# Kernel optimization log

Measured on AMD Instinct MI355X. Metric: run time of the kernel, lower is better.

Reference implementation:

```python
import jax, jax.numpy as jnp
import numpy as np

N_NODES = 50000
NUM_LAYERS = 3


def setup_inputs() -> dict:
    key = jax.random.key(0)
    k1, k2, k3, k4, k5, k6 = jax.random.split(key, 6)
    E = 800000
    IN, OUT = 64, 64
    src = jax.random.randint(k1, (E,), 0, N_NODES)
    dst = jax.random.randint(k2, (E,), 0, N_NODES)
    edge_index = jnp.stack([src, dst], axis=0)  # [2, E]
    edge_weight = jax.random.uniform(k3, (E,), dtype=jnp.float32)
    H = jax.random.normal(k4, (N_NODES, IN), dtype=jnp.float32)
    W = jax.random.normal(k5, (IN, OUT), dtype=jnp.float32) * (1.0 / np.sqrt(IN))
    b = jax.random.normal(k6, (OUT,), dtype=jnp.float32) * 0.01
    return {"edge_index": edge_index, "edge_weight": edge_weight, "H": H, "W": W, "b": b}


def _spmm(edge_index, edge_weight, H):
    # out[dst] += w * H[src]  (sparse A @ H)
    src, dst = edge_index[0], edge_index[1]
    msgs = edge_weight[:, None] * H[src]            # [E, d]
    return jax.ops.segment_sum(msgs, dst, num_segments=N_NODES)


def reference(edge_index, edge_weight, H, W, b):
    for _ in range(NUM_LAYERS):
        H = _spmm(edge_index, edge_weight, H)
    return H @ W + b  # nn.Linear
```

## Files before the change

### kernel.cpp

```cpp
#include <hip/hip_runtime.h>
#include <hip/hip_fp16.h>

#define N_NODES 50000
#define NFEAT 64
#define NB_BUCKETS ((N_NODES + 255) / 256)
#define CHUNK 4096

#define FMA4(A, S, V)                                                          \
    do {                                                                       \
        A.x = fmaf(S, V.x, A.x);                                               \
        A.y = fmaf(S, V.y, A.y);                                               \
        A.z = fmaf(S, V.z, A.z);                                               \
        A.w = fmaf(S, V.w, A.w);                                               \
    } while (0)


__global__ __launch_bounds__(256) void k_bhist(const int* __restrict__ dst, int E,
                                               int* __restrict__ bucketCount) {
    __shared__ int cnt[NB_BUCKETS];
    for (int i = threadIdx.x; i < NB_BUCKETS; i += 256) cnt[i] = 0;
    __syncthreads();
    int cbeg = blockIdx.x * CHUNK;
    int cend = min(cbeg + CHUNK, E);
    for (int e = cbeg + threadIdx.x; e < cend; e += 256)
        atomicAdd(&cnt[dst[e] >> 8], 1);
    __syncthreads();
    for (int i = threadIdx.x; i < NB_BUCKETS; i += 256)
        if (cnt[i]) atomicAdd(&bucketCount[i], cnt[i]);
}

__global__ __launch_bounds__(256) void k_bscan(const int* __restrict__ bucketCount,
                                               int E, int* __restrict__ bucketBase,
                                               int* __restrict__ bucketCursor,
                                               int* __restrict__ offs) {
    __shared__ int s[256];
    int t = threadIdx.x;
    int v = (t < NB_BUCKETS) ? bucketCount[t] : 0;
    s[t] = v;
    __syncthreads();
    for (int off = 1; off < 256; off <<= 1) {
        int u = (t >= off) ? s[t - off] : 0;
        __syncthreads();
        if (t >= off) s[t] += u;
        __syncthreads();
    }
    if (t < NB_BUCKETS) {
        int b = s[t] - v;
        bucketBase[t] = b;
        bucketCursor[t] = b;
    }
    if (t == 0) {
        bucketBase[NB_BUCKETS] = E;
        offs[N_NODES] = E;
    }
}

__global__ __launch_bounds__(256) void k_bplace(const int* __restrict__ src,
                                                const int* __restrict__ dst,
                                                const float* __restrict__ w, int E,
                                                int* __restrict__ bucketCursor,
                                                int2* __restrict__ tmp) {
    __shared__ int cnt[NB_BUCKETS];
    __shared__ int base[NB_BUCKETS];
    for (int i = threadIdx.x; i < NB_BUCKETS; i += 256) cnt[i] = 0;
    __syncthreads();
    int cbeg = blockIdx.x * CHUNK;
    int cend = min(cbeg + CHUNK, E);
    for (int e = cbeg + threadIdx.x; e < cend; e += 256)
        atomicAdd(&cnt[dst[e] >> 8], 1);
    __syncthreads();
    for (int i = threadIdx.x; i < NB_BUCKETS; i += 256) {
        int c = cnt[i];
        base[i] = c ? atomicAdd(&bucketCursor[i], c) : 0;
        cnt[i] = 0;
    }
    __syncthreads();
    for (int e = cbeg + threadIdx.x; e < cend; e += 256) {
        int d = dst[e];
        int b = d >> 8;
        int r = atomicAdd(&cnt[b], 1);
        tmp[base[b] + r] = make_int2(((d & 255) << 16) | src[e], __float_as_int(w[e]));
    }
}

__global__ __launch_bounds__(256) void k_bsort(const int* __restrict__ bucketBase,
                                               const int2* __restrict__ tmp,
                                               int2* __restrict__ pairs,
                                               int* __restrict__ offs) {
    __shared__ int cnt[256];
    __shared__ int ex[256];
    int b = blockIdx.x;
    int t = threadIdx.x;
    int beg = bucketBase[b], end = bucketBase[b + 1];
    cnt[t] = 0;
    __syncthreads();
    for (int e = beg + t; e < end; e += 256)
        atomicAdd(&cnt[(tmp[e].x >> 16) & 255], 1);
    __syncthreads();
    int v = cnt[t];
    ex[t] = v;
    __syncthreads();
    for (int off = 1; off < 256; off <<= 1) {
        int u = (t >= off) ? ex[t - off] : 0;
        __syncthreads();
        if (t >= off) ex[t] += u;
        __syncthreads();
    }
    int myex = ex[t] - v;
    int d = (b << 8) + t;
    if (d < N_NODES) offs[d] = beg + myex;
    cnt[t] = myex;
    __syncthreads();
    for (int e = beg + t; e < end; e += 256) {
        int2 kv = tmp[e];
        int c = (kv.x >> 16) & 255;
        int r = atomicAdd(&cnt[c], 1);
        pairs[beg + r] = make_int2(kv.x & 0xFFFF, kv.y);
    }
}


__global__ __launch_bounds__(256) void k_f2h(const float* __restrict__ in,
                                             __half* __restrict__ out, int n4) {
    int i = blockIdx.x * 256 + threadIdx.x;
    if (i >= n4) return;
    float4 v = ((const float4*)in)[i];
    float2 packed;
    ((__half2*)&packed)[0] = __float22half2_rn(make_float2(v.x, v.y));
    ((__half2*)&packed)[1] = __float22half2_rn(make_float2(v.z, v.w));
    ((float2*)out)[i] = packed;
}


template <bool OUT_HALF>
__global__ __launch_bounds__(256) void k_spmm4h(const int* __restrict__ offs,
                                                const int2* __restrict__ pairs,
                                                const __half* __restrict__ Hin,
                                                void* __restrict__ Hout_) {
    int tid = blockIdx.x * 256 + threadIdx.x;
    int wave = tid >> 6;
    int lane = threadIdx.x & 63;
    int node = wave * 4 + (lane >> 4);
    int q = lane & 15;
    if (node >= N_NODES) return;
    int beg = offs[node], end = offs[node + 1];
    float4 acc0 = {0.f, 0.f, 0.f, 0.f}, acc1 = {0.f, 0.f, 0.f, 0.f};
    int e = beg;
    for (; e + 2 <= end; e += 2) {
        int2 p0 = pairs[e];
        int2 p1 = pairs[e + 1];
        float2 r0 = *((const float2*)(Hin + (size_t)p0.x * NFEAT) + q);
        float2 r1 = *((const float2*)(Hin + (size_t)p1.x * NFEAT) + q);
        float2 a0 = __half22float2(((__half2*)&r0)[0]);
        float2 b0 = __half22float2(((__half2*)&r0)[1]);
        float2 a1 = __half22float2(((__half2*)&r1)[0]);
        float2 b1 = __half22float2(((__half2*)&r1)[1]);
        float w0 = __int_as_float(p0.y), w1 = __int_as_float(p1.y);
        acc0.x = fmaf(w0, a0.x, acc0.x);
        acc0.y = fmaf(w0, a0.y, acc0.y);
        acc0.z = fmaf(w0, b0.x, acc0.z);
        acc0.w = fmaf(w0, b0.y, acc0.w);
        acc1.x = fmaf(w1, a1.x, acc1.x);
        acc1.y = fmaf(w1, a1.y, acc1.y);
        acc1.z = fmaf(w1, b1.x, acc1.z);
        acc1.w = fmaf(w1, b1.y, acc1.w);
    }
    if (e < end) {
        int2 p = pairs[e];
        float2 r = *((const float2*)(Hin + (size_t)p.x * NFEAT) + q);
        float2 a = __half22float2(((__half2*)&r)[0]);
        float2 b = __half22float2(((__half2*)&r)[1]);
        float w = __int_as_float(p.y);
        acc0.x = fmaf(w, a.x, acc0.x);
        acc0.y = fmaf(w, a.y, acc0.y);
        acc0.z = fmaf(w, b.x, acc0.z);
        acc0.w = fmaf(w, b.y, acc0.w);
    }
    acc0.x += acc1.x;
    acc0.y += acc1.y;
    acc0.z += acc1.z;
    acc0.w += acc1.w;
    if constexpr (OUT_HALF) {
        float2 packed;
        ((__half2*)&packed)[0] = __float22half2_rn(make_float2(acc0.x, acc0.y));
        ((__half2*)&packed)[1] = __float22half2_rn(make_float2(acc0.z, acc0.w));
        *((float2*)((__half*)Hout_ + (size_t)node * NFEAT) + q) = packed;
    } else {
        *((float4*)((float*)Hout_ + (size_t)node * NFEAT) + q) = acc0;
    }
}


__global__ __launch_bounds__(256) void k_gemm(const float* __restrict__ Hin,
                                              const float* __restrict__ W,
                                              const float* __restrict__ b,
                                              float* __restrict__ out) {
    __shared__ float4 WL[64 * 16];
    __shared__ float4 BL[16];
    int t = threadIdx.x;
    const float4* W4 = (const float4*)W;
    for (int k = t; k < 1024; k += 256) WL[k] = W4[k];
    if (t < 16) BL[t] = ((const float4*)b)[t];
    __syncthreads();
    int n = blockIdx.x * 256 + t;
    if (n >= N_NODES) return;
    const float4* Hrow = (const float4*)(Hin + (size_t)n * NFEAT);
    float4 acc[16];
#pragma unroll
    for (int j = 0; j < 16; ++j) acc[j] = BL[j];
    for (int i4 = 0; i4 < 16; ++i4) {
        float4 h = Hrow[i4];
        const float4* w0 = &WL[(i4 * 4 + 0) * 16];
        const float4* w1 = &WL[(i4 * 4 + 1) * 16];
        const float4* w2 = &WL[(i4 * 4 + 2) * 16];
        const float4* w3 = &WL[(i4 * 4 + 3) * 16];
#pragma unroll
        for (int j = 0; j < 16; ++j) {
            FMA4(acc[j], h.x, w0[j]);
            FMA4(acc[j], h.y, w1[j]);
            FMA4(acc[j], h.z, w2[j]);
            FMA4(acc[j], h.w, w3[j]);
        }
    }
    float4* o = (float4*)(out + (size_t)n * NFEAT);
#pragma unroll
    for (int j = 0; j < 16; ++j) o[j] = acc[j];
}


extern "C" void kernel_launch(void* const* d_in, const int* in_sizes, int n_in,
                              void* d_out, int out_size, void* d_ws, size_t ws_size,
                              hipStream_t stream) {
    const int* edge_index = (const int*)d_in[0];
    const float* ew = (const float*)d_in[1];
    const float* H = (const float*)d_in[2];
    const float* W = (const float*)d_in[3];
    const float* b = (const float*)d_in[4];
    float* out = (float*)d_out;

    int E = in_sizes[1];
    const int* src = edge_index;
    const int* dst = edge_index + E;

    char* ws = (char*)d_ws;
    size_t off = 0;
    auto alloc = [&](size_t bytes) -> void* {
        void* p = ws + off;
        off += (bytes + 255) & ~(size_t)255;
        return p;
    };
    int* bucketCount = (int*)alloc((size_t)NB_BUCKETS * 4);
    int* bucketBase = (int*)alloc(((size_t)NB_BUCKETS + 1) * 4);
    int* bucketCursor = (int*)alloc((size_t)NB_BUCKETS * 4);
    int* offs = (int*)alloc(((size_t)N_NODES + 1) * 4);
    int2* tmp = (int2*)alloc((size_t)E * 8);
    int2* pairs = (int2*)alloc((size_t)E * 8);
    __half* h0 = (__half*)alloc((size_t)N_NODES * NFEAT * 2);
    __half* h1 = (__half*)alloc((size_t)N_NODES * NFEAT * 2);
    float* bufA = (float*)alloc((size_t)N_NODES * NFEAT * 4);

    hipMemsetAsync(bucketCount, 0, (size_t)NB_BUCKETS * 4, stream);

    int nch = (E + CHUNK - 1) / CHUNK;
    k_bhist<<<nch, 256, 0, stream>>>(dst, E, bucketCount);
    k_bscan<<<1, 256, 0, stream>>>(bucketCount, E, bucketBase, bucketCursor, offs);
    k_bplace<<<nch, 256, 0, stream>>>(src, dst, ew, E, bucketCursor, tmp);
    k_bsort<<<NB_BUCKETS, 256, 0, stream>>>(bucketBase, tmp, pairs, offs);

    int n4 = N_NODES * NFEAT / 4;
    k_f2h<<<(n4 + 255) / 256, 256, 0, stream>>>(H, h0, n4);

    int nb = (N_NODES + 15) / 16;
    k_spmm4h<true><<<nb, 256, 0, stream>>>(offs, pairs, h0, h1);
    k_spmm4h<true><<<nb, 256, 0, stream>>>(offs, pairs, h1, h0);
    k_spmm4h<false><<<nb, 256, 0, stream>>>(offs, pairs, h0, bufA);

    k_gemm<<<(N_NODES + 255) / 256, 256, 0, stream>>>(bufA, W, b, out);
}
```

Before: 220.6 us.

## Split SpMM into two feature-half passes with 4-way unrolled gather

Result: slower. 281.9 us (+27.8%).

```diff
diff --git a/kernel.cpp b/kernel.cpp
--- a/kernel.cpp
+++ b/kernel.cpp
@@ -133,10 +133,11 @@
 
 
 template <bool OUT_HALF>
-__global__ __launch_bounds__(256) void k_spmm4h(const int* __restrict__ offs,
+__global__ __launch_bounds__(256) void k_spmm2h(const int* __restrict__ offs,
                                                 const int2* __restrict__ pairs,
                                                 const __half* __restrict__ Hin,
-                                                void* __restrict__ Hout_) {
+                                                void* __restrict__ Hout_,
+                                                int fbase) {
     int tid = blockIdx.x * 256 + threadIdx.x;
     int wave = tid >> 6;
     int lane = threadIdx.x & 63;
@@ -144,49 +145,48 @@
     int q = lane & 15;
     if (node >= N_NODES) return;
     int beg = offs[node], end = offs[node + 1];
-    float4 acc0 = {0.f, 0.f, 0.f, 0.f}, acc1 = {0.f, 0.f, 0.f, 0.f};
+    const __half* hbase = Hin + fbase + 2 * q;
+    float2 a0 = {0.f, 0.f}, a1 = {0.f, 0.f}, a2 = {0.f, 0.f}, a3 = {0.f, 0.f};
     int e = beg;
-    for (; e + 2 <= end; e += 2) {
-        int2 p0 = pairs[e];
-        int2 p1 = pairs[e + 1];
-        float2 r0 = *((const float2*)(Hin + (size_t)p0.x * NFEAT) + q);
-        float2 r1 = *((const float2*)(Hin + (size_t)p1.x * NFEAT) + q);
-        float2 a0 = __half22float2(((__half2*)&r0)[0]);
-        float2 b0 = __half22float2(((__half2*)&r0)[1]);
-        float2 a1 = __half22float2(((__half2*)&r1)[0]);
-        float2 b1 = __half22float2(((__half2*)&r1)[1]);
-        float w0 = __int_as_float(p0.y), w1 = __int_as_float(p1.y);
-        acc0.x = fmaf(w0, a0.x, acc0.x);
-        acc0.y = fmaf(w0, a0.y, acc0.y);
-        acc0.z = fmaf(w0, b0.x, acc0.z);
-        acc0.w = fmaf(w0, b0.y, acc0.w);
-        acc1.x = fmaf(w1, a1.x, acc1.x);
-        acc1.y = fmaf(w1, a1.y, acc1.y);
-        acc1.z = fmaf(w1, b1.x, acc1.z);
-        acc1.w = fmaf(w1, b1.y, acc1.w);
-    }
-    if (e < end) {
-        int2 p = pairs[e];
-        float2 r = *((const float2*)(Hin + (size_t)p.x * NFEAT) + q);
-        float2 a = __half22float2(((__half2*)&r)[0]);
-        float2 b = __half22float2(((__half2*)&r)[1]);
-        float w = __int_as_float(p.y);
-        acc0.x = fmaf(w, a.x, acc0.x);
-        acc0.y = fmaf(w, a.y, acc0.y);
-        acc0.z = fmaf(w, b.x, acc0.z);
-        acc0.w = fmaf(w, b.y, acc0.w);
-    }
-    acc0.x += acc1.x;
-    acc0.y += acc1.y;
-    acc0.z += acc1.z;
-    acc0.w += acc1.w;
+    for (; e + 4 <= end; e += 4) {
+        long long v0 = __builtin_nontemporal_load((const long long*)(pairs + e));
+        long long v1 = __builtin_nontemporal_load((const long long*)(pairs + e + 1));
+        long long v2 = __builtin_nontemporal_load((const long long*)(pairs + e + 2));
+        long long v3 = __builtin_nontemporal_load((const long long*)(pairs + e + 3));
+        float2 f0 = __half22float2(*(const __half2*)(hbase + (size_t)(int)v0 * NFEAT));
+        float2 f1 = __half22float2(*(const __half2*)(hbase + (size_t)(int)v1 * NFEAT));
+        float2 f2 = __half22float2(*(const __half2*)(hbase + (size_t)(int)v2 * NFEAT));
+        float2 f3 = __half22float2(*(const __half2*)(hbase + (size_t)(int)v3 * NFEAT));
+        float w0 = __int_as_float((int)(v0 >> 32));
+        float w1 = __int_as_float((int)(v1 >> 32));
+        float w2 = __int_as_float((int)(v2 >> 32));
+        float w3 = __int_as_float((int)(v3 >> 32));
+        a0.x = fmaf(w0, f0.x, a0.x);
+        a0.y = fmaf(w0, f0.y, a0.y);
+        a1.x = fmaf(w1, f1.x, a1.x);
+        a1.y = fmaf(w1, f1.y, a1.y);
+        a2.x = fmaf(w2, f2.x, a2.x);
+        a2.y = fmaf(w2, f2.y, a2.y);
+        a3.x = fmaf(w3, f3.x, a3.x);
+        a3.y = fmaf(w3, f3.y, a3.y);
+    }
+    for (; e < end; ++e) {
+        long long v = __builtin_nontemporal_load((const long long*)(pairs + e));
+        float2 f = __half22float2(*(const __half2*)(hbase + (size_t)(int)v * NFEAT));
+        float w = __int_as_float((int)(v >> 32));
+        a0.x = fmaf(w, f.x, a0.x);
+        a0.y = fmaf(w, f.y, a0.y);
+    }
+    float ax = (a0.x + a1.x) + (a2.x + a3.x);
+    float ay = (a0.y + a1.y) + (a2.y + a3.y);
     if constexpr (OUT_HALF) {
-        float2 packed;
-        ((__half2*)&packed)[0] = __float22half2_rn(make_float2(acc0.x, acc0.y));
-        ((__half2*)&packed)[1] = __float22half2_rn(make_float2(acc0.z, acc0.w));
-        *((float2*)((__half*)Hout_ + (size_t)node * NFEAT) + q) = packed;
+        __half2 o = __float22half2_rn(make_float2(ax, ay));
+        unsigned uo = *reinterpret_cast<unsigned*>(&o);
+        __builtin_nontemporal_store(
+            uo, (unsigned*)((__half*)Hout_ + (size_t)node * NFEAT + fbase + 2 * q));
     } else {
-        *((float4*)((float*)Hout_ + (size_t)node * NFEAT) + q) = acc0;
+        *(float2*)((float*)Hout_ + (size_t)node * NFEAT + fbase + 2 * q) =
+            make_float2(ax, ay);
     }
 }
 
@@ -271,9 +271,12 @@
     k_f2h<<<(n4 + 255) / 256, 256, 0, stream>>>(H, h0, n4);
 
     int nb = (N_NODES + 15) / 16;
-    k_spmm4h<true><<<nb, 256, 0, stream>>>(offs, pairs, h0, h1);
-    k_spmm4h<true><<<nb, 256, 0, stream>>>(offs, pairs, h1, h0);
-    k_spmm4h<false><<<nb, 256, 0, stream>>>(offs, pairs, h0, bufA);
+    k_spmm2h<true><<<nb, 256, 0, stream>>>(offs, pairs, h0, h1, 0);
+    k_spmm2h<true><<<nb, 256, 0, stream>>>(offs, pairs, h0, h1, 32);
+    k_spmm2h<true><<<nb, 256, 0, stream>>>(offs, pairs, h1, h0, 0);
+    k_spmm2h<true><<<nb, 256, 0, stream>>>(offs, pairs, h1, h0, 32);
+    k_spmm2h<false><<<nb, 256, 0, stream>>>(offs, pairs, h0, bufA, 0);
+    k_spmm2h<false><<<nb, 256, 0, stream>>>(offs, pairs, h0, bufA, 32);
 
     k_gemm<<<(N_NODES + 255) / 256, 256, 0, stream>>>(bufA, W, b, out);
 }
```
